# Kernel tuning notes

Measured on AMD Instinct MI355X. Metric: run time of the kernel, lower is better.

## Reference

```python
import jax, jax.numpy as jnp
import numpy as np

TS = 0.01  # Euler step size (module's `ts`)

N_X, N_U, N_FEAT = 32, 16, 512
BATCH, SEQ_LEN = 512, 2048


def setup_inputs() -> dict:
    key = jax.random.key(0)
    k0, k1, k2, k3 = jax.random.split(key, 4)
    x0_batch = jax.random.normal(k0, (BATCH, 1, N_X), dtype=jnp.float32)
    u_batch = jax.random.normal(k1, (BATCH, SEQ_LEN, N_U), dtype=jnp.float32)
    # 2-layer MLP state-space model: Linear(n_x+n_u, n_feat) -> Tanh -> Linear(n_feat, n_x)
    fan1 = N_X + N_U
    W1 = jax.random.normal(k2, (fan1, N_FEAT), dtype=jnp.float32) / np.sqrt(fan1).astype(np.float32)
    b1 = jnp.zeros((N_FEAT,), dtype=jnp.float32)
    W2 = jax.random.normal(k3, (N_FEAT, N_X), dtype=jnp.float32) / np.sqrt(N_FEAT).astype(np.float32)
    b2 = jnp.zeros((N_X,), dtype=jnp.float32)
    return {"x0_batch": x0_batch, "u_batch": u_batch, "W1": W1, "b1": b1, "W2": W2, "b2": b2}


def reference(x0_batch, u_batch, W1, b1, W2, b2):
    # x0_batch: (B, 1, n_x); u_batch: (B, T, n_u) -> out: (B, T, n_x)
    x0 = x0_batch[:, 0, :]                       # (B, n_x)
    u_t = jnp.swapaxes(u_batch, 0, 1)            # (T, B, n_u) for scan over time

    def step(x, u):
        h = jnp.tanh(jnp.concatenate([x, u], axis=-1) @ W1 + b1)  # (B, n_feat)
        dx = h @ W2 + b2                                           # (B, n_x)
        x_next = x + TS * dx
        return x_next, x_next

    _, xs = jax.lax.scan(step, x0, u_t)          # xs: (T, B, n_x)
    return jnp.swapaxes(xs, 0, 1)                # (B, T, n_x)
```

## Files before the change

kernel.cpp:

```cpp
#include <hip/hip_runtime.h>

typedef float v2f __attribute__((ext_vector_type(2)));
typedef unsigned uv2 __attribute__((ext_vector_type(2)));

constexpr int NX = 32, NU = 16, NF = 512;
constexpr int SEQ = 2048;
constexpr int NT = 256;
constexpr float SC  = 2.88539008177792681f;
constexpr float TSC = 0.01f;

template<int CTRL>
__device__ __forceinline__ float dpp_mov(float v) {
    return __int_as_float(__builtin_amdgcn_update_dpp(0, __float_as_int(v), CTRL, 0xF, 0xF, true));
}
__device__ __forceinline__ float sum16(float v) {
    uv2 r = __builtin_amdgcn_permlane16_swap(__float_as_uint(v), __float_as_uint(v), false, false);
    return __uint_as_float(r.x) + __uint_as_float(r.y);
}
__device__ __forceinline__ float sum32(float v) {
    uv2 r = __builtin_amdgcn_permlane32_swap(__float_as_uint(v), __float_as_uint(v), false, false);
    return __uint_as_float(r.x) + __uint_as_float(r.y);
}

__device__ __forceinline__ float tanh4(float y) {
    const float e = __builtin_amdgcn_exp2f(y);
    const float r = __builtin_amdgcn_rcpf(e + 1.f);
    return fmaf(-2.f, r, 1.f);
}

__device__ __forceinline__ void bar_lds() {
    asm volatile("s_waitcnt lgkmcnt(0)" ::: "memory");
    __builtin_amdgcn_sched_barrier(0);
    __builtin_amdgcn_s_barrier();
    __builtin_amdgcn_sched_barrier(0);
    asm volatile("" ::: "memory");
}

__global__ __launch_bounds__(NT)
__attribute__((amdgpu_waves_per_eu(2, 2)))
void fes_kernel(const float* __restrict__ x0, const float* __restrict__ ug,
                const float* __restrict__ W1, const float* __restrict__ b1,
                const float* __restrict__ W2, const float* __restrict__ b2,
                float* __restrict__ out)
{
    __shared__ __align__(16) float xs_w[4][NX];
    __shared__ float part[2][8][33];

    const int tid = threadIdx.x, row = blockIdx.x;
    const int l = tid & 63, w = tid >> 6;

    const int pi = ((l & 1) << 4) | (((l >> 1) & 1) << 3) | (((l >> 3) & 1) << 2)
                 | (((l >> 4) & 1) << 1) | ((l >> 5) & 1);
    const int slot = w * 2 + ((l >> 2) & 1);
    const bool jown = (l & 4) == 0;
    const bool store_lane = (w == 0) && jown;

    const int f0 = 2 * tid, f1 = f0 + 1;

    v2f wkA[24], wkB[24];
#pragma unroll
    for (int p = 0; p < 24; ++p) {
        wkA[p] = v2f{SC * W1[(2 * p) * NF + f0], SC * W1[(2 * p + 1) * NF + f0]};
        wkB[p] = v2f{SC * W1[(2 * p) * NF + f1], SC * W1[(2 * p + 1) * NF + f1]};
    }
    const float b1A = SC * b1[f0], b1B = SC * b1[f1];

    v2f wcA[16], wcB[16];
#pragma unroll
    for (int m = 0; m < 16; ++m) {
        wcA[m] = v2f{TSC * W2[f0 * NX + ((2 * m) ^ pi)], TSC * W2[f0 * NX + ((2 * m + 1) ^ pi)]};
        wcB[m] = v2f{TSC * W2[f1 * NX + ((2 * m) ^ pi)], TSC * W2[f1 * NX + ((2 * m + 1) ^ pi)]};
    }
    const float bb = TSC * b2[pi];
    float xr = x0[row * NX + pi];

    const float* ug_row  = ug  + (size_t)row * SEQ * NU;
    float*       out_row = out + (size_t)row * SEQ * NX;

    if (jown) xs_w[w][pi] = xr;
    float4 u0 = *(const float4*)(ug_row + 0);
    float4 u1 = *(const float4*)(ug_row + 4);
    float4 u2 = *(const float4*)(ug_row + 8);
    float4 u3 = *(const float4*)(ug_row + 12);

    const float4* xsr = (const float4*)xs_w[w];

#pragma unroll 1
    for (int t = 0; t < SEQ; ++t) {
        v2f aA0 = {b1A, 0.f}, aA1 = {0.f, 0.f};
        v2f aB0 = {b1B, 0.f}, aB1 = {0.f, 0.f};
#pragma unroll
        for (int s = 0; s < 8; ++s) {
            const float4 iv = xsr[s];
            const v2f lo = {iv.x, iv.y}, hi = {iv.z, iv.w};
            aA0 += wkA[2 * s] * lo;  aA1 += wkA[2 * s + 1] * hi;
            aB0 += wkB[2 * s] * lo;  aB1 += wkB[2 * s + 1] * hi;
        }
#define UPART(uv, p0)                                                       \
        { const v2f lo = {uv.x, uv.y}, hi = {uv.z, uv.w};                   \
          aA0 += wkA[p0] * lo;  aA1 += wkA[p0 + 1] * hi;                    \
          aB0 += wkB[p0] * lo;  aB1 += wkB[p0 + 1] * hi; }
        UPART(u0, 16) UPART(u1, 18) UPART(u2, 20) UPART(u3, 22)
#undef UPART
        {
            const int tn = (t + 1 < SEQ) ? t + 1 : SEQ - 1;
            const float* un = ug_row + (size_t)tn * NU;
            u0 = *(const float4*)(un + 0);
            u1 = *(const float4*)(un + 4);
            u2 = *(const float4*)(un + 8);
            u3 = *(const float4*)(un + 12);
        }
        const float h0 = tanh4((aA0.x + aA0.y) + (aA1.x + aA1.y));
        const float h1 = tanh4((aB0.x + aB0.y) + (aB1.x + aB1.y));

        const v2f h0v = {h0, h0}, h1v = {h1, h1};
        v2f q[16];
#pragma unroll
        for (int m = 0; m < 16; ++m)
            q[m] = h0v * wcA[m] + h1v * wcB[m];

#pragma unroll
        for (int m = 0; m < 8; ++m) {
            q[m].x += dpp_mov<0xB1>(q[m + 8].x);
            q[m].y += dpp_mov<0xB1>(q[m + 8].y);
        }
#pragma unroll
        for (int m = 0; m < 4; ++m) {
            q[m].x += dpp_mov<0x4E>(q[m + 4].x);
            q[m].y += dpp_mov<0x4E>(q[m + 4].y);
        }
#pragma unroll
        for (int m = 0; m < 2; ++m) {
            q[m].x += dpp_mov<0x128>(q[m + 2].x);
            q[m].y += dpp_mov<0x128>(q[m + 2].y);
        }
        const float S0 = q[0].x + (sum16(q[1].x) - q[1].x);
        const float S1 = q[0].y + (sum16(q[1].y) - q[1].y);
        const float S = S0 + (sum32(S1) - S1);

        part[t & 1][slot][pi] = S;
        bar_lds();
        const float* pb = &part[t & 1][0][pi];
        const float p0 = pb[0],   p1 = pb[33],  p2 = pb[66],  p3 = pb[99];
        const float p4 = pb[132], p5 = pb[165], p6 = pb[198], p7 = pb[231];
        const float dx = (((p0 + p1) + (p2 + p3)) + ((p4 + p5) + (p6 + p7))) + bb;
        const float xn = xr + dx;
        xr = xn;
        if (store_lane) out_row[(size_t)t * NX + pi] = xn;
        if (jown) xs_w[w][pi] = xn;
    }
}

extern "C" void kernel_launch(void* const* d_in, const int* in_sizes, int n_in,
                              void* d_out, int out_size, void* d_ws, size_t ws_size,
                              hipStream_t stream) {
    const float* x0 = (const float*)d_in[0];
    const float* ug = (const float*)d_in[1];
    const float* W1 = (const float*)d_in[2];
    const float* b1 = (const float*)d_in[3];
    const float* W2 = (const float*)d_in[4];
    const float* b2 = (const float*)d_in[5];
    float* out = (float*)d_out;

    fes_kernel<<<dim3(512), dim3(NT), 0, stream>>>(x0, ug, W1, b1, W2, b2, out);
}
```

Before: 1.742 ms.

## Broadcast new state via readlane into SGPRs instead of LDS round-trip

The updated state vector used to be written to a per-wave LDS buffer and read back as float4 each step. Now every lane computes it redundantly and it is broadcast to 32 scalar values with v_readlane, so the x part of the first layer runs as scalar-operand FMAs with no LDS read. The partial-sum buffer is also transposed so each lane reads its 8 partials as two float4 loads instead of eight strided loads. In exchange, the 32 readlanes sit serially on the critical path each step, and the first-layer FMAs are no longer packed, which adds VALU instructions.

```diff
diff --git a/kernel.cpp b/kernel.cpp
--- a/kernel.cpp
+++ b/kernel.cpp
@@ -43,25 +43,30 @@
                 const float* __restrict__ W2, const float* __restrict__ b2,
                 float* __restrict__ out)
 {
-    __shared__ __align__(16) float xs_w[4][NX];
-    __shared__ float part[2][8][33];
+    __shared__ __align__(16) float part[2][NX][12];
 
     const int tid = threadIdx.x, row = blockIdx.x;
     const int l = tid & 63, w = tid >> 6;
 
     const int pi = ((l & 1) << 4) | (((l >> 1) & 1) << 3) | (((l >> 3) & 1) << 2)
                  | (((l >> 4) & 1) << 1) | ((l >> 5) & 1);
-    const int slot = w * 2 + ((l >> 2) & 1);
-    const bool jown = (l & 4) == 0;
-    const bool store_lane = (w == 0) && jown;
+    const int slot = 2 * w + ((l >> 2) & 1);
+    const bool store_lane = (w == 0) && ((l & 4) == 0);
 
     const int f0 = 2 * tid, f1 = f0 + 1;
 
-    v2f wkA[24], wkB[24];
+    float w1A[32], w1B[32];
 #pragma unroll
-    for (int p = 0; p < 24; ++p) {
-        wkA[p] = v2f{SC * W1[(2 * p) * NF + f0], SC * W1[(2 * p + 1) * NF + f0]};
-        wkB[p] = v2f{SC * W1[(2 * p) * NF + f1], SC * W1[(2 * p + 1) * NF + f1]};
+    for (int k = 0; k < 32; ++k) {
+        w1A[k] = SC * W1[k * NF + f0];
+        w1B[k] = SC * W1[k * NF + f1];
+    }
+    v2f wuA[8], wuB[8];
+#pragma unroll
+    for (int p = 0; p < 8; ++p) {
+        const int k = NX + 2 * p;
+        wuA[p] = v2f{SC * W1[k * NF + f0], SC * W1[(k + 1) * NF + f0]};
+        wuB[p] = v2f{SC * W1[k * NF + f1], SC * W1[(k + 1) * NF + f1]};
     }
     const float b1A = SC * b1[f0], b1B = SC * b1[f1];
 
@@ -74,34 +79,40 @@
     const float bb = TSC * b2[pi];
     float xr = x0[row * NX + pi];
 
+    float xu[32];
+#pragma unroll
+    for (int k = 0; k < 32; ++k) xu[k] = x0[row * NX + k];
+
     const float* ug_row  = ug  + (size_t)row * SEQ * NU;
     float*       out_row = out + (size_t)row * SEQ * NX;
 
-    if (jown) xs_w[w][pi] = xr;
     float4 u0 = *(const float4*)(ug_row + 0);
     float4 u1 = *(const float4*)(ug_row + 4);
     float4 u2 = *(const float4*)(ug_row + 8);
     float4 u3 = *(const float4*)(ug_row + 12);
 
-    const float4* xsr = (const float4*)xs_w[w];
-
 #pragma unroll 1
     for (int t = 0; t < SEQ; ++t) {
-        v2f aA0 = {b1A, 0.f}, aA1 = {0.f, 0.f};
-        v2f aB0 = {b1B, 0.f}, aB1 = {0.f, 0.f};
+        float aA0 = b1A, aA1 = 0.f, aA2 = 0.f, aA3 = 0.f;
+        float aB0 = b1B, aB1 = 0.f, aB2 = 0.f, aB3 = 0.f;
 #pragma unroll
-        for (int s = 0; s < 8; ++s) {
-            const float4 iv = xsr[s];
-            const v2f lo = {iv.x, iv.y}, hi = {iv.z, iv.w};
-            aA0 += wkA[2 * s] * lo;  aA1 += wkA[2 * s + 1] * hi;
-            aB0 += wkB[2 * s] * lo;  aB1 += wkB[2 * s + 1] * hi;
+        for (int k = 0; k < 32; k += 4) {
+            aA0 = fmaf(w1A[k],     xu[k],     aA0);
+            aA1 = fmaf(w1A[k + 1], xu[k + 1], aA1);
+            aA2 = fmaf(w1A[k + 2], xu[k + 2], aA2);
+            aA3 = fmaf(w1A[k + 3], xu[k + 3], aA3);
+            aB0 = fmaf(w1B[k],     xu[k],     aB0);
+            aB1 = fmaf(w1B[k + 1], xu[k + 1], aB1);
+            aB2 = fmaf(w1B[k + 2], xu[k + 2], aB2);
+            aB3 = fmaf(w1B[k + 3], xu[k + 3], aB3);
         }
-#define UPART(uv, p0)                                                       \
+        v2f uA = {0.f, 0.f}, uB = {0.f, 0.f};
+#define UPAIR(uv, p)                                                        \
         { const v2f lo = {uv.x, uv.y}, hi = {uv.z, uv.w};                   \
-          aA0 += wkA[p0] * lo;  aA1 += wkA[p0 + 1] * hi;                    \
-          aB0 += wkB[p0] * lo;  aB1 += wkB[p0 + 1] * hi; }
-        UPART(u0, 16) UPART(u1, 18) UPART(u2, 20) UPART(u3, 22)
-#undef UPART
+          uA += wuA[p] * lo;  uA += wuA[p + 1] * hi;                        \
+          uB += wuB[p] * lo;  uB += wuB[p + 1] * hi; }
+        UPAIR(u0, 0) UPAIR(u1, 2) UPAIR(u2, 4) UPAIR(u3, 6)
+#undef UPAIR
         {
             const int tn = (t + 1 < SEQ) ? t + 1 : SEQ - 1;
             const float* un = ug_row + (size_t)tn * NU;
@@ -110,8 +121,8 @@
             u2 = *(const float4*)(un + 8);
             u3 = *(const float4*)(un + 12);
         }
-        const float h0 = tanh4((aA0.x + aA0.y) + (aA1.x + aA1.y));
-        const float h1 = tanh4((aB0.x + aB0.y) + (aB1.x + aB1.y));
+        const float h0 = tanh4(((aA0 + aA1) + (aA2 + aA3)) + (uA.x + uA.y));
+        const float h1 = tanh4(((aB0 + aB1) + (aB2 + aB3)) + (uB.x + uB.y));
 
         const v2f h0v = {h0, h0}, h1v = {h1, h1};
         v2f q[16];
@@ -136,18 +147,24 @@
         }
         const float S0 = q[0].x + (sum16(q[1].x) - q[1].x);
         const float S1 = q[0].y + (sum16(q[1].y) - q[1].y);
-        const float S = S0 + (sum32(S1) - S1);
+        const float S  = S0 + (sum32(S1) - S1);
 
-        part[t & 1][slot][pi] = S;
+        part[t & 1][pi][slot] = S;
         bar_lds();
-        const float* pb = &part[t & 1][0][pi];
-        const float p0 = pb[0],   p1 = pb[33],  p2 = pb[66],  p3 = pb[99];
-        const float p4 = pb[132], p5 = pb[165], p6 = pb[198], p7 = pb[231];
-        const float dx = (((p0 + p1) + (p2 + p3)) + ((p4 + p5) + (p6 + p7))) + bb;
+        const float4 pa = *(const float4*)&part[t & 1][pi][0];
+        const float4 pb4 = *(const float4*)&part[t & 1][pi][4];
+        const float dx = (((pa.x + pa.y) + (pa.z + pa.w))
+                        + ((pb4.x + pb4.y) + (pb4.z + pb4.w))) + bb;
         const float xn = xr + dx;
         xr = xn;
         if (store_lane) out_row[(size_t)t * NX + pi] = xn;
-        if (jown) xs_w[w][pi] = xn;
+
+#pragma unroll
+        for (int k = 0; k < 32; ++k) {
+            const int L = ((k >> 4) & 1) | (((k >> 3) & 1) << 1) | (((k >> 2) & 1) << 3)
+                        | (((k >> 1) & 1) << 4) | ((k & 1) << 5);
+            xu[k] = __int_as_float(__builtin_amdgcn_readlane(__float_as_int(xn), L));
+        }
     }
 }
 
```

Measured after the change: 1.979 ms. 1.14x slower.

## Halve block to 128 threads with four hidden features per thread

Applied to the files above, without the earlier changes.

Each block now runs 128 threads, and each thread owns four hidden units instead of two. The W1 and W2 register tiles double and occupancy is set to one wave per EU. With two waves instead of four per block, the cross-wave partial sums shrink to four slots per output, so they are read with one float4 LDS load. The barrier also synchronises fewer waves. The trade is roughly twice the per-thread FMA work on the serial critical path and higher register pressure, with less latency hiding.

```diff
diff --git a/kernel.cpp b/kernel.cpp
--- a/kernel.cpp
+++ b/kernel.cpp
@@ -5,7 +5,7 @@
 
 constexpr int NX = 32, NU = 16, NF = 512;
 constexpr int SEQ = 2048;
-constexpr int NT = 256;
+constexpr int NT = 128;
 constexpr float SC  = 2.88539008177792681f;
 constexpr float TSC = 0.01f;
 
@@ -37,40 +37,44 @@
 }
 
 __global__ __launch_bounds__(NT)
-__attribute__((amdgpu_waves_per_eu(2, 2)))
+__attribute__((amdgpu_waves_per_eu(1, 1)))
 void fes_kernel(const float* __restrict__ x0, const float* __restrict__ ug,
                 const float* __restrict__ W1, const float* __restrict__ b1,
                 const float* __restrict__ W2, const float* __restrict__ b2,
                 float* __restrict__ out)
 {
-    __shared__ __align__(16) float xs_w[4][NX];
-    __shared__ float part[2][8][33];
+    __shared__ __align__(16) float xs_w[2][NX];
+    __shared__ __align__(16) float part[2][NX][12];
 
     const int tid = threadIdx.x, row = blockIdx.x;
     const int l = tid & 63, w = tid >> 6;
 
     const int pi = ((l & 1) << 4) | (((l >> 1) & 1) << 3) | (((l >> 3) & 1) << 2)
                  | (((l >> 4) & 1) << 1) | ((l >> 5) & 1);
-    const int slot = w * 2 + ((l >> 2) & 1);
+    const int slot = 2 * w + ((l >> 2) & 1);
     const bool jown = (l & 4) == 0;
     const bool store_lane = (w == 0) && jown;
 
-    const int f0 = 2 * tid, f1 = f0 + 1;
+    const int fb = 4 * tid;
 
-    v2f wkA[24], wkB[24];
+    v2f wk[4][24];
 #pragma unroll
-    for (int p = 0; p < 24; ++p) {
-        wkA[p] = v2f{SC * W1[(2 * p) * NF + f0], SC * W1[(2 * p + 1) * NF + f0]};
-        wkB[p] = v2f{SC * W1[(2 * p) * NF + f1], SC * W1[(2 * p + 1) * NF + f1]};
-    }
-    const float b1A = SC * b1[f0], b1B = SC * b1[f1];
+    for (int c = 0; c < 4; ++c)
+#pragma unroll
+        for (int p = 0; p < 24; ++p)
+            wk[c][p] = v2f{SC * W1[(2 * p) * NF + fb + c],
+                           SC * W1[(2 * p + 1) * NF + fb + c]};
+    float b1r[4];
+#pragma unroll
+    for (int c = 0; c < 4; ++c) b1r[c] = SC * b1[fb + c];
 
-    v2f wcA[16], wcB[16];
+    v2f wc[4][16];
 #pragma unroll
-    for (int m = 0; m < 16; ++m) {
-        wcA[m] = v2f{TSC * W2[f0 * NX + ((2 * m) ^ pi)], TSC * W2[f0 * NX + ((2 * m + 1) ^ pi)]};
-        wcB[m] = v2f{TSC * W2[f1 * NX + ((2 * m) ^ pi)], TSC * W2[f1 * NX + ((2 * m + 1) ^ pi)]};
-    }
+    for (int c = 0; c < 4; ++c)
+#pragma unroll
+        for (int m = 0; m < 16; ++m)
+            wc[c][m] = v2f{TSC * W2[(fb + c) * NX + ((2 * m) ^ pi)],
+                           TSC * W2[(fb + c) * NX + ((2 * m + 1) ^ pi)]};
     const float bb = TSC * b2[pi];
     float xr = x0[row * NX + pi];
 
@@ -87,21 +91,28 @@
 
 #pragma unroll 1
     for (int t = 0; t < SEQ; ++t) {
-        v2f aA0 = {b1A, 0.f}, aA1 = {0.f, 0.f};
-        v2f aB0 = {b1B, 0.f}, aB1 = {0.f, 0.f};
+        v2f ae[4], ao[4];
+#pragma unroll
+        for (int c = 0; c < 4; ++c) { ae[c] = v2f{b1r[c], 0.f}; ao[c] = v2f{0.f, 0.f}; }
 #pragma unroll
         for (int s = 0; s < 8; ++s) {
             const float4 iv = xsr[s];
             const v2f lo = {iv.x, iv.y}, hi = {iv.z, iv.w};
-            aA0 += wkA[2 * s] * lo;  aA1 += wkA[2 * s + 1] * hi;
-            aB0 += wkB[2 * s] * lo;  aB1 += wkB[2 * s + 1] * hi;
+#pragma unroll
+            for (int c = 0; c < 4; ++c) {
+                ae[c] += wk[c][2 * s] * lo;
+                ao[c] += wk[c][2 * s + 1] * hi;
+            }
         }
-#define UPART(uv, p0)                                                       \
-        { const v2f lo = {uv.x, uv.y}, hi = {uv.z, uv.w};                   \
-          aA0 += wkA[p0] * lo;  aA1 += wkA[p0 + 1] * hi;                    \
-          aB0 += wkB[p0] * lo;  aB1 += wkB[p0 + 1] * hi; }
-        UPART(u0, 16) UPART(u1, 18) UPART(u2, 20) UPART(u3, 22)
-#undef UPART
+#define UQ(uv, qd)                                                          \
+        {   const v2f lo = {uv.x, uv.y}, hi = {uv.z, uv.w};                 \
+            _Pragma("unroll")                                               \
+            for (int c = 0; c < 4; ++c) {                                   \
+                ae[c] += wk[c][16 + 2 * (qd)] * lo;                         \
+                ao[c] += wk[c][17 + 2 * (qd)] * hi;                         \
+            } }
+        UQ(u0, 0) UQ(u1, 1) UQ(u2, 2) UQ(u3, 3)
+#undef UQ
         {
             const int tn = (t + 1 < SEQ) ? t + 1 : SEQ - 1;
             const float* un = ug_row + (size_t)tn * NU;
@@ -110,14 +121,20 @@
             u2 = *(const float4*)(un + 8);
             u3 = *(const float4*)(un + 12);
         }
-        const float h0 = tanh4((aA0.x + aA0.y) + (aA1.x + aA1.y));
-        const float h1 = tanh4((aB0.x + aB0.y) + (aB1.x + aB1.y));
+        float h[4];
+#pragma unroll
+        for (int c = 0; c < 4; ++c)
+            h[c] = tanh4((ae[c].x + ae[c].y) + (ao[c].x + ao[c].y));
 
-        const v2f h0v = {h0, h0}, h1v = {h1, h1};
         v2f q[16];
 #pragma unroll
-        for (int m = 0; m < 16; ++m)
-            q[m] = h0v * wcA[m] + h1v * wcB[m];
+        for (int m = 0; m < 16; ++m) {
+            v2f acc = v2f{h[0], h[0]} * wc[0][m];
+            acc += v2f{h[1], h[1]} * wc[1][m];
+            acc += v2f{h[2], h[2]} * wc[2][m];
+            acc += v2f{h[3], h[3]} * wc[3][m];
+            q[m] = acc;
+        }
 
 #pragma unroll
         for (int m = 0; m < 8; ++m) {
@@ -136,15 +153,12 @@
         }
         const float S0 = q[0].x + (sum16(q[1].x) - q[1].x);
         const float S1 = q[0].y + (sum16(q[1].y) - q[1].y);
-        const float S = S0 + (sum32(S1) - S1);
+        const float S  = S0 + (sum32(S1) - S1);
 
-        part[t & 1][slot][pi] = S;
+        part[t & 1][pi][slot] = S;
         bar_lds();
-        const float* pb = &part[t & 1][0][pi];
-        const float p0 = pb[0],   p1 = pb[33],  p2 = pb[66],  p3 = pb[99];
-        const float p4 = pb[132], p5 = pb[165], p6 = pb[198], p7 = pb[231];
-        const float dx = (((p0 + p1) + (p2 + p3)) + ((p4 + p5) + (p6 + p7))) + bb;
-        const float xn = xr + dx;
+        const float4 pv = *(const float4*)&part[t & 1][pi][0];
+        const float xn = xr + ((pv.x + pv.y) + (pv.z + pv.w)) + bb;
         xr = xn;
         if (store_lane) out_row[(size_t)t * NX + pi] = xn;
         if (jown) xs_w[w][pi] = xn;
```

After: 2.453 ms. 40.8% more time.

## Process two batch rows per block to share weights and barriers

Applied to the files above, without the earlier changes.

Each block now advances two independent batch rows through the recurrence, reusing the register-resident W1/W2 slices for both and using a single LDS barrier per time step for both rows. The grid is halved and the occupancy hint drops to one wave per EU, replacing hardware wave interleaving with instruction-level interleaving of two independent chains. Scheduling barriers around the s_barrier are removed to give the compiler freedom. Risk is longer per-step critical path and fewer resident waves to hide latency.

```diff
diff --git a/kernel.cpp b/kernel.cpp
--- a/kernel.cpp
+++ b/kernel.cpp
@@ -30,30 +30,28 @@
 
 __device__ __forceinline__ void bar_lds() {
     asm volatile("s_waitcnt lgkmcnt(0)" ::: "memory");
-    __builtin_amdgcn_sched_barrier(0);
     __builtin_amdgcn_s_barrier();
-    __builtin_amdgcn_sched_barrier(0);
     asm volatile("" ::: "memory");
 }
 
 __global__ __launch_bounds__(NT)
-__attribute__((amdgpu_waves_per_eu(2, 2)))
+__attribute__((amdgpu_waves_per_eu(1, 1)))
 void fes_kernel(const float* __restrict__ x0, const float* __restrict__ ug,
                 const float* __restrict__ W1, const float* __restrict__ b1,
                 const float* __restrict__ W2, const float* __restrict__ b2,
                 float* __restrict__ out)
 {
-    __shared__ __align__(16) float xs_w[4][NX];
-    __shared__ float part[2][8][33];
-
-    const int tid = threadIdx.x, row = blockIdx.x;
+    __shared__ __align__(16) float xs_w[4][2][NX];
+    __shared__ float part[2][2][8][33];
+
+    const int tid = threadIdx.x;
+    const int rowA = 2 * blockIdx.x, rowB = rowA + 1;
     const int l = tid & 63, w = tid >> 6;
 
     const int pi = ((l & 1) << 4) | (((l >> 1) & 1) << 3) | (((l >> 3) & 1) << 2)
                  | (((l >> 4) & 1) << 1) | ((l >> 5) & 1);
-    const int slot = w * 2 + ((l >> 2) & 1);
+    const int slot = 2 * w + ((l >> 2) & 1);
     const bool jown = (l & 4) == 0;
-    const bool store_lane = (w == 0) && jown;
 
     const int f0 = 2 * tid, f1 = f0 + 1;
 
@@ -72,82 +70,148 @@
         wcB[m] = v2f{TSC * W2[f1 * NX + ((2 * m) ^ pi)], TSC * W2[f1 * NX + ((2 * m + 1) ^ pi)]};
     }
     const float bb = TSC * b2[pi];
-    float xr = x0[row * NX + pi];
-
-    const float* ug_row  = ug  + (size_t)row * SEQ * NU;
-    float*       out_row = out + (size_t)row * SEQ * NX;
-
-    if (jown) xs_w[w][pi] = xr;
-    float4 u0 = *(const float4*)(ug_row + 0);
-    float4 u1 = *(const float4*)(ug_row + 4);
-    float4 u2 = *(const float4*)(ug_row + 8);
-    float4 u3 = *(const float4*)(ug_row + 12);
-
-    const float4* xsr = (const float4*)xs_w[w];
+
+    float xrA = x0[rowA * NX + pi];
+    float xrB = x0[rowB * NX + pi];
+
+    const float* ugA  = ug  + (size_t)rowA * SEQ * NU;
+    const float* ugB  = ug  + (size_t)rowB * SEQ * NU;
+    float*       outA = out + (size_t)rowA * SEQ * NX;
+    float*       outB = out + (size_t)rowB * SEQ * NX;
+
+    if (jown) {
+        xs_w[w][0][pi] = xrA;
+        xs_w[w][1][pi] = xrB;
+    }
+    const float4* xsA = (const float4*)xs_w[w][0];
+    const float4* xsB = (const float4*)xs_w[w][1];
+
+    float4 uA0 = *(const float4*)(ugA + 0), uA1 = *(const float4*)(ugA + 4);
+    float4 uA2 = *(const float4*)(ugA + 8), uA3 = *(const float4*)(ugA + 12);
+    float4 uB0 = *(const float4*)(ugB + 0), uB1 = *(const float4*)(ugB + 4);
+    float4 uB2 = *(const float4*)(ugB + 8), uB3 = *(const float4*)(ugB + 12);
 
 #pragma unroll 1
     for (int t = 0; t < SEQ; ++t) {
-        v2f aA0 = {b1A, 0.f}, aA1 = {0.f, 0.f};
-        v2f aB0 = {b1B, 0.f}, aB1 = {0.f, 0.f};
+        v2f pA0 = {b1A, 0.f}, pA1 = {0.f, 0.f};
+        v2f qA0 = {b1B, 0.f}, qA1 = {0.f, 0.f};
 #pragma unroll
         for (int s = 0; s < 8; ++s) {
-            const float4 iv = xsr[s];
+            const float4 iv = xsA[s];
             const v2f lo = {iv.x, iv.y}, hi = {iv.z, iv.w};
-            aA0 += wkA[2 * s] * lo;  aA1 += wkA[2 * s + 1] * hi;
-            aB0 += wkB[2 * s] * lo;  aB1 += wkB[2 * s + 1] * hi;
-        }
-#define UPART(uv, p0)                                                       \
+            pA0 += wkA[2 * s] * lo;  pA1 += wkA[2 * s + 1] * hi;
+            qA0 += wkB[2 * s] * lo;  qA1 += wkB[2 * s + 1] * hi;
+        }
+#define UPART(uv, p0, pe, po, qe, qo)                                       \
         { const v2f lo = {uv.x, uv.y}, hi = {uv.z, uv.w};                   \
-          aA0 += wkA[p0] * lo;  aA1 += wkA[p0 + 1] * hi;                    \
-          aB0 += wkB[p0] * lo;  aB1 += wkB[p0 + 1] * hi; }
-        UPART(u0, 16) UPART(u1, 18) UPART(u2, 20) UPART(u3, 22)
+          pe += wkA[p0] * lo;  po += wkA[p0 + 1] * hi;                      \
+          qe += wkB[p0] * lo;  qo += wkB[p0 + 1] * hi; }
+        UPART(uA0, 16, pA0, pA1, qA0, qA1)
+        UPART(uA1, 18, pA0, pA1, qA0, qA1)
+        UPART(uA2, 20, pA0, pA1, qA0, qA1)
+        UPART(uA3, 22, pA0, pA1, qA0, qA1)
+        const float h0A = tanh4((pA0.x + pA0.y) + (pA1.x + pA1.y));
+        const float h1A = tanh4((qA0.x + qA0.y) + (qA1.x + qA1.y));
+
+        v2f pB0 = {b1A, 0.f}, pB1 = {0.f, 0.f};
+        v2f qB0 = {b1B, 0.f}, qB1 = {0.f, 0.f};
+#pragma unroll
+        for (int s = 0; s < 8; ++s) {
+            const float4 iv = xsB[s];
+            const v2f lo = {iv.x, iv.y}, hi = {iv.z, iv.w};
+            pB0 += wkA[2 * s] * lo;  pB1 += wkA[2 * s + 1] * hi;
+            qB0 += wkB[2 * s] * lo;  qB1 += wkB[2 * s + 1] * hi;
+        }
+        UPART(uB0, 16, pB0, pB1, qB0, qB1)
+        UPART(uB1, 18, pB0, pB1, qB0, qB1)
+        UPART(uB2, 20, pB0, pB1, qB0, qB1)
+        UPART(uB3, 22, pB0, pB1, qB0, qB1)
 #undef UPART
+        const float h0B = tanh4((pB0.x + pB0.y) + (pB1.x + pB1.y));
+        const float h1B = tanh4((qB0.x + qB0.y) + (qB1.x + qB1.y));
+
+        float SA;
+        {
+            const v2f h0v = {h0A, h0A}, h1v = {h1A, h1A};
+            v2f r[16];
+#pragma unroll
+            for (int m = 0; m < 16; ++m) r[m] = h0v * wcA[m] + h1v * wcB[m];
+#pragma unroll
+            for (int m = 0; m < 8; ++m) {
+                r[m].x += dpp_mov<0xB1>(r[m + 8].x);
+                r[m].y += dpp_mov<0xB1>(r[m + 8].y);
+            }
+#pragma unroll
+            for (int m = 0; m < 4; ++m) {
+                r[m].x += dpp_mov<0x4E>(r[m + 4].x);
+                r[m].y += dpp_mov<0x4E>(r[m + 4].y);
+            }
+#pragma unroll
+            for (int m = 0; m < 2; ++m) {
+                r[m].x += dpp_mov<0x128>(r[m + 2].x);
+                r[m].y += dpp_mov<0x128>(r[m + 2].y);
+            }
+            const float S0 = r[0].x + (sum16(r[1].x) - r[1].x);
+            const float S1 = r[0].y + (sum16(r[1].y) - r[1].y);
+            SA = S0 + (sum32(S1) - S1);
+        }
+        part[t & 1][0][slot][pi] = SA;
+
+        float SB;
+        {
+            const v2f h0v = {h0B, h0B}, h1v = {h1B, h1B};
+            v2f r[16];
+#pragma unroll
+            for (int m = 0; m < 16; ++m) r[m] = h0v * wcA[m] + h1v * wcB[m];
+#pragma unroll
+            for (int m = 0; m < 8; ++m) {
+                r[m].x += dpp_mov<0xB1>(r[m + 8].x);
+                r[m].y += dpp_mov<0xB1>(r[m + 8].y);
+            }
+#pragma unroll
+            for (int m = 0; m < 4; ++m) {
+                r[m].x += dpp_mov<0x4E>(r[m + 4].x);
+                r[m].y += dpp_mov<0x4E>(r[m + 4].y);
+            }
+#pragma unroll
+            for (int m = 0; m < 2; ++m) {
+                r[m].x += dpp_mov<0x128>(r[m + 2].x);
+                r[m].y += dpp_mov<0x128>(r[m + 2].y);
+            }
+            const float S0 = r[0].x + (sum16(r[1].x) - r[1].x);
+            const float S1 = r[0].y + (sum16(r[1].y) - r[1].y);
+            SB = S0 + (sum32(S1) - S1);
+        }
+        part[t & 1][1][slot][pi] = SB;
+
         {
             const int tn = (t + 1 < SEQ) ? t + 1 : SEQ - 1;
-            const float* un = ug_row + (size_t)tn * NU;
-            u0 = *(const float4*)(un + 0);
-            u1 = *(const float4*)(un + 4);
-            u2 = *(const float4*)(un + 8);
-            u3 = *(const float4*)(un + 12);
-        }
-        const float h0 = tanh4((aA0.x + aA0.y) + (aA1.x + aA1.y));
-        const float h1 = tanh4((aB0.x + aB0.y) + (aB1.x + aB1.y));
-
-        const v2f h0v = {h0, h0}, h1v = {h1, h1};
-        v2f q[16];
-#pragma unroll
-        for (int m = 0; m < 16; ++m)
-            q[m] = h0v * wcA[m] + h1v * wcB[m];
-
-#pragma unroll
-        for (int m = 0; m < 8; ++m) {
-            q[m].x += dpp_mov<0xB1>(q[m + 8].x);
-            q[m].y += dpp_mov<0xB1>(q[m + 8].y);
-        }
-#pragma unroll
-        for (int m = 0; m < 4; ++m) {
-            q[m].x += dpp_mov<0x4E>(q[m + 4].x);
-            q[m].y += dpp_mov<0x4E>(q[m + 4].y);
-        }
-#pragma unroll
-        for (int m = 0; m < 2; ++m) {
-            q[m].x += dpp_mov<0x128>(q[m + 2].x);
-            q[m].y += dpp_mov<0x128>(q[m + 2].y);
-        }
-        const float S0 = q[0].x + (sum16(q[1].x) - q[1].x);
-        const float S1 = q[0].y + (sum16(q[1].y) - q[1].y);
-        const float S = S0 + (sum32(S1) - S1);
-
-        part[t & 1][slot][pi] = S;
+            const float* unA = ugA + (size_t)tn * NU;
+            const float* unB = ugB + (size_t)tn * NU;
+            uA0 = *(const float4*)(unA + 0);  uA1 = *(const float4*)(unA + 4);
+            uA2 = *(const float4*)(unA + 8);  uA3 = *(const float4*)(unA + 12);
+            uB0 = *(const float4*)(unB + 0);  uB1 = *(const float4*)(unB + 4);
+            uB2 = *(const float4*)(unB + 8);  uB3 = *(const float4*)(unB + 12);
+        }
+
         bar_lds();
-        const float* pb = &part[t & 1][0][pi];
-        const float p0 = pb[0],   p1 = pb[33],  p2 = pb[66],  p3 = pb[99];
-        const float p4 = pb[132], p5 = pb[165], p6 = pb[198], p7 = pb[231];
-        const float dx = (((p0 + p1) + (p2 + p3)) + ((p4 + p5) + (p6 + p7))) + bb;
-        const float xn = xr + dx;
-        xr = xn;
-        if (store_lane) out_row[(size_t)t * NX + pi] = xn;
-        if (jown) xs_w[w][pi] = xn;
+
+        const float* pa = &part[t & 1][0][0][pi];
+        const float a0 = pa[0],   a1 = pa[33],  a2 = pa[66],  a3 = pa[99];
+        const float a4 = pa[132], a5 = pa[165], a6 = pa[198], a7 = pa[231];
+        const float* pbq = &part[t & 1][1][0][pi];
+        const float c0 = pbq[0],   c1 = pbq[33],  c2 = pbq[66],  c3 = pbq[99];
+        const float c4 = pbq[132], c5 = pbq[165], c6 = pbq[198], c7 = pbq[231];
+        const float xnA = xrA + ((((a0 + a1) + (a2 + a3)) + ((a4 + a5) + (a6 + a7))) + bb);
+        const float xnB = xrB + ((((c0 + c1) + (c2 + c3)) + ((c4 + c5) + (c6 + c7))) + bb);
+        xrA = xnA; xrB = xnB;
+
+        if (w == 0 && jown) outA[(size_t)t * NX + pi] = xnA;
+        if (w == 1 && jown) outB[(size_t)t * NX + pi] = xnB;
+        if (jown) {
+            xs_w[w][0][pi] = xnA;
+            xs_w[w][1][pi] = xnB;
+        }
     }
 }
 
@@ -162,5 +226,5 @@
     const float* b2 = (const float*)d_in[5];
     float* out = (float*)d_out;
 
-    fes_kernel<<<dim3(512), dim3(NT), 0, stream>>>(x0, ug, W1, b1, W2, b2, out);
-}
+    fes_kernel<<<dim3(256), dim3(NT), 0, stream>>>(x0, ug, W1, b1, W2, b2, out);
+}
```

Measured after the change: 2.541 ms. 45.9% more time.
